# Kernel tuning notes

Measured on AMD Instinct MI355X. Metric: run time of the kernel, lower is better.

## Reference

```python
import jax, jax.numpy as jnp
import numpy as np

SLICES = (512, 32, 0, 8, 40, 72, 104, 136, 168, 200, 232, 264, 296)


def _build_params(slices):
    (d_in, w_pos, st_, sym1_, sym2_, pos1_, pos2_, pos3_,
     scr1_, scr2_, scr3_, scr4_, scr5_) = slices
    w_q = np.zeros((w_pos + 1, d_in), np.float32)
    b_q = -np.ones(w_pos + 1, np.float32)
    w_q[np.arange(w_pos), pos3_ + np.arange(w_pos)] = 2.0
    b_q[w_pos] = 1.0
    w_k = np.zeros((w_pos + 1, d_in), np.float32)
    b_k = -np.ones(w_pos + 1, np.float32)
    w_k[np.arange(w_pos), pos1_ + np.arange(w_pos)] = 2.0
    b_k[w_pos] = 0.0
    w_v = np.zeros((d_in, d_in), np.float32)
    b_v = np.zeros(d_in, np.float32)
    n = scr3_ - scr2_
    w_v[scr2_ + np.arange(n), sym1_ + np.arange(n)] = 1.0
    b_v[scr4_ + 1] = 1.0
    k_0 = np.zeros(w_pos + 1, np.float32)
    k_0[w_pos] = float(w_pos - 1)
    v_0 = np.zeros(d_in, np.float32)
    return {k: jnp.asarray(v) for k, v in dict(
        w_q=w_q, b_q=b_q, w_k=w_k, b_k=b_k, w_v=w_v, b_v=b_v,
        k_0=k_0, v_0=v_0).items()}


def setup_inputs() -> dict:
    key = jax.random.key(0)
    k1, k2 = jax.random.split(key)
    B, T, S, d_in = 8, 2048, 2048, SLICES[0]
    inp = {
        'tgt': jax.random.normal(k1, (B, T, d_in), dtype=jnp.float32),
        'memory': jax.random.normal(k2, (B, S, d_in), dtype=jnp.float32),
    }
    inp.update(_build_params(SLICES))
    return inp


def reference(tgt, memory, w_q, b_q, w_k, b_k, w_v, b_v, k_0, v_0):
    # Single-head cross-attention with an extra constant (k_0, v_0) token,
    # followed by a residual add (tgt += attn_out).
    B = tgt.shape[0]
    q = tgt @ w_q.T + b_q            # [B, T, h]   h = w_pos + 1
    k = memory @ w_k.T + b_k         # [B, S, h]
    v = memory @ w_v.T + b_v         # [B, S, d_in]
    # prepend the fixed default key/value token
    k0 = jnp.broadcast_to(k_0, (B, 1, k_0.shape[0]))
    v0 = jnp.broadcast_to(v_0, (B, 1, v_0.shape[0]))
    k = jnp.concatenate([k0, k], axis=1)   # [B, S+1, h]
    v = jnp.concatenate([v0, v], axis=1)   # [B, S+1, d_in]
    scores = jnp.einsum('bth,bsh->bts', q, k)      # [B, T, S+1]
    attn = jax.nn.softmax(scores, axis=-1)
    out = jnp.einsum('bts,bsd->btd', attn, v)       # [B, T, d_in]
    return tgt + out
```

## Files before the change

kernel.cpp:

```cpp
#include <hip/hip_runtime.h>
#include <hip/hip_bf16.h>

#define B_   8
#define T_   2048
#define S_   2048
#define DIN  512
#define QOFF 136
#define KOFF 72
#define VSRC 8

typedef __attribute__((ext_vector_type(8))) short    bf16x8;
typedef __attribute__((ext_vector_type(8))) _Float16 f16x8;
typedef __attribute__((ext_vector_type(4))) float    f32x4;

constexpr int KSEC = 0;
constexpr int VSEC = 524288;
constexpr int BATCH_U = 65536;

constexpr int BLK = 256;
constexpr int NGW = 16;

__device__ __forceinline__ ushort f2b(float x) {
  __hip_bfloat16 h = __float2bfloat16(x);
  return __builtin_bit_cast(ushort, h);
}
__device__ __forceinline__ ushort f2h(float x) {
  return __builtin_bit_cast(ushort, (_Float16)x);
}

__global__ __launch_bounds__(256)
void preproc(const float* __restrict__ mem, ushort* __restrict__ ws) {
  const int t    = threadIdx.x;
  const int b    = blockIdx.x >> 5;
  const int key0 = (blockIdx.x & 31) * 64;
  const float*  mbase = mem + (size_t)b * S_ * DIN;
  ushort* wk = ws + KSEC + (size_t)b * BATCH_U;
  ushort* wv = ws + VSEC + (size_t)b * BATCH_U;

  #pragma unroll
  for (int rep = 0; rep < 2; ++rep) {
    const int cid = t + 256 * rep;
    const int key = cid >> 3, c = cid & 7;
    const float4 k4 = *(const float4*)(mbase + (size_t)(key0 + key) * DIN + KOFF + 4 * c);
    const float kf[4] = {k4.x, k4.y, k4.z, k4.w};
    ushort kh[4];
    #pragma unroll
    for (int e = 0; e < 4; ++e) kh[e] = f2h(2.f * kf[e] - 1.f);
    const int gkey = key0 + key;
    const int pos  = (gkey >> 4) * 512 + ((gkey & 15) + 16 * (c >> 1)) * 8 + 4 * (c & 1);
    *(uint2*)(wk + pos) = *(const uint2*)kh;
  }

  const int ch = t & 31, h = t >> 5;
  float vv[8];
  #pragma unroll
  for (int r = 0; r < 8; ++r)
    vv[r] = mbase[(size_t)(key0 + 8 * h + r) * DIN + VSRC + ch];
  ushort vb[8];
  #pragma unroll
  for (int r = 0; r < 8; ++r) vb[r] = f2b(vv[r]);
  #pragma unroll
  for (int half = 0; half < 2; ++half) {
    const int key = key0 + 8 * h + 4 * half;
    const int pos = (key >> 5) * 1024 + (ch >> 4) * 512
                  + ((ch & 15) + 16 * ((key >> 2) & 3)) * 8 + ((key >> 4) & 1) * 4;
    *(uint2*)(wv + pos) = *(const uint2*)&vb[half * 4];
  }
}

__device__ __forceinline__ void mwrite(float* d, int lane, float m, float ls,
                                       const f32x4& o0, const f32x4& o1) {
  d[lane] = m;
  d[64 + lane] = ls;
  #pragma unroll
  for (int i = 0; i < 4; ++i) {
    d[128 + i * 64 + lane] = o0[i];
    d[384 + i * 64 + lane] = o1[i];
  }
}
__device__ __forceinline__ void mread(const float* s, int lane, float& m,
                                      float& ls, f32x4& o0, f32x4& o1) {
  const float m1 = s[lane], l1 = s[64 + lane];
  const float mn = fmaxf(m, m1);
  const float sa = __expf(m - mn), sb = __expf(m1 - mn);
  ls = ls * sa + l1 * sb;
  #pragma unroll
  for (int i = 0; i < 4; ++i) {
    o0[i] = o0[i] * sa + s[128 + i * 64 + lane] * sb;
    o1[i] = o1[i] * sa + s[384 + i * 64 + lane] * sb;
  }
  m = mn;
}

__global__ __launch_bounds__(BLK, 4)
void attn_main(const float* __restrict__ tgt, const ushort* __restrict__ ws,
               float* __restrict__ out) {
  __shared__ float msl[3 * 640 + 561];

  const int tid  = threadIdx.x;
  const int lane = tid & 63;
  const int wv   = tid >> 6;
  const int Q    = lane >> 4;
  const int r15  = lane & 15;

  const int o  = (blockIdx.x & 7) * 128 + (blockIdx.x >> 3);
  const int b  = o >> 7;
  const int t0 = (o & 127) * 16;

  const ushort* wsK = ws + KSEC + (size_t)b * BATCH_U;
  const ushort* wsV = ws + VSEC + (size_t)b * BATCH_U;
  const size_t  base = (size_t)(b * T_ + t0) * DIN;

  const float* tr = tgt + base + (size_t)r15 * DIN + QOFF + 8 * Q;
  const float4 qa = *(const float4*)tr;
  const float4 qb = *(const float4*)(tr + 4);
  f16x8 pf;
  {
    const float pv[8] = {qa.x, qa.y, qa.z, qa.w, qb.x, qb.y, qb.z, qb.w};
    #pragma unroll
    for (int e = 0; e < 8; ++e) pf[e] = (_Float16)(2.f * pv[e] - 1.f);
  }

  float m  = 31.f;
  float ls = (Q == 0 && wv == 0) ? 1.f : 0.f;
  f32x4 oc0 = {0.f, 0.f, 0.f, 0.f}, oc1 = {0.f, 0.f, 0.f, 0.f};

  bf16x8 stg[2][4];
  #define ISSUE(g, pb)                                                         \
    { const int ki = (wv * 32 + 2 * (g)) * 512 + lane * 8;                     \
      stg[pb][0] = *(const bf16x8*)(wsK + ki);                                 \
      stg[pb][1] = *(const bf16x8*)(wsK + ki + 512);                           \
      const int vi = (wv * NGW + (g)) * 1024 + lane * 8;                       \
      stg[pb][2] = *(const bf16x8*)(wsV + vi);                                 \
      stg[pb][3] = *(const bf16x8*)(wsV + vi + 512); }

  f32x4 cp[2];
  int cpr[2], cpc[2];
  #define CLOAD(c, pb)                                                         \
    { const int vid = (c) * BLK + tid;                                         \
      cpr[pb] = vid >> 7; cpc[pb] = vid & 127;                                 \
      cp[pb] = *(const f32x4*)(tgt + base + (size_t)cpr[pb] * DIN + cpc[pb] * 4); }
  #define CSTORE(pb)                                                           \
    { const int cc = cpc[pb];                                                  \
      if (!((cc >= 50 && cc < 58) || cc == 66))                                \
        *(f32x4*)(out + base + (size_t)cpr[pb] * DIN + cc * 4) = cp[pb]; }

  ISSUE(0, 0)
  ISSUE(1, 1)
  CLOAD(0, 0)

  #pragma unroll
  for (int g = 0; g < NGW; ++g) {
    const int pb = g & 1;
    if (g >= 1 && g <= 8) CSTORE((g - 1) & 1)
    if (g >= 1 && g < 8)  CLOAD(g, g & 1)

    const f16x8  k0 = __builtin_bit_cast(f16x8, stg[pb][0]);
    const f16x8  k1 = __builtin_bit_cast(f16x8, stg[pb][1]);
    const bf16x8 v0 = stg[pb][2];
    const bf16x8 v1 = stg[pb][3];

    f32x4 c0 = {0.f, 0.f, 0.f, 0.f}, c1 = {0.f, 0.f, 0.f, 0.f};
    c0 = __builtin_amdgcn_mfma_f32_16x16x32_f16(k0, pf, c0, 0, 0, 0);
    c1 = __builtin_amdgcn_mfma_f32_16x16x32_f16(k1, pf, c1, 0, 0, 0);

    if (g + 2 < NGW) ISSUE(g + 2, pb)

    float gm = fmaxf(fmaxf(fmaxf(c0[0], c0[1]), fmaxf(c0[2], c0[3])),
                     fmaxf(fmaxf(c1[0], c1[1]), fmaxf(c1[2], c1[3])));
    gm = fmaxf(gm, __shfl_xor(gm, 16));
    gm = fmaxf(gm, __shfl_xor(gm, 32));
    if (__any(gm > m + 8.f)) {
      const float mn  = gm;
      const float scl = __expf(m - fmaxf(m, mn));
      const float mx  = fmaxf(m, mn);
      m = mx;
      ls *= scl;
      #pragma unroll
      for (int i = 0; i < 4; ++i) { oc0[i] *= scl; oc1[i] *= scl; }
    }

    bf16x8 wf;
    float wsum = 0.f;
    #pragma unroll
    for (int j = 0; j < 8; ++j) {
      const float w = __expf(((j < 4) ? c0[j & 3] : c1[j & 3]) - m);
      wsum += w;
      wf[j] = (short)f2b(w);
    }
    ls += wsum;

    oc0 = __builtin_amdgcn_mfma_f32_16x16x32_bf16(v0, wf, oc0, 0, 0, 0);
    oc1 = __builtin_amdgcn_mfma_f32_16x16x32_bf16(v1, wf, oc1, 0, 0, 0);
  }
  #undef ISSUE
  #undef CLOAD
  #undef CSTORE

  if (wv >= 2) mwrite(msl + (wv - 2) * 640, lane, m, ls, oc0, oc1);
  __syncthreads();
  if (wv < 2) mread(msl + wv * 640, lane, m, ls, oc0, oc1);
  __syncthreads();
  if (wv == 1) mwrite(msl, lane, m, ls, oc0, oc1);
  __syncthreads();
  float* olds = msl + 1920;
  if (wv == 0) {
    mread(msl, lane, m, ls, oc0, oc1);
    float t2 = ls + __shfl_xor(ls, 16);
    const float lt  = t2 + __shfl_xor(t2, 32);
    const float inv = 1.f / lt;
    #pragma unroll
    for (int i = 0; i < 4; ++i) {
      olds[(4 * Q + i) * 17 + r15]      = oc0[i] * inv;
      olds[(16 + 4 * Q + i) * 17 + r15] = oc1[i] * inv;
    }
    if (Q == 0) olds[32 * 17 + r15] = 1.f - __expf(31.f - m) * inv;
  }
  __syncthreads();

  if (tid < 144) {
    const int row = tid / 9, j = tid - row * 9;
    const int c4i = (j < 8) ? (50 + j) : 66;
    const size_t off = base + (size_t)row * DIN + c4i * 4;
    float4 ov = *(const float4*)(tgt + off);
    if (j < 8) {
      ov.x += olds[(4 * j + 0) * 17 + row];
      ov.y += olds[(4 * j + 1) * 17 + row];
      ov.z += olds[(4 * j + 2) * 17 + row];
      ov.w += olds[(4 * j + 3) * 17 + row];
    } else {
      ov.y += olds[32 * 17 + row];
    }
    *(float4*)(out + off) = ov;
  }
}

extern "C" void kernel_launch(void* const* d_in, const int* in_sizes, int n_in,
                              void* d_out, int out_size, void* d_ws, size_t ws_size,
                              hipStream_t stream) {
  const float* tgt = (const float*)d_in[0];
  const float* mem = (const float*)d_in[1];
  ushort* ws = (ushort*)d_ws;
  float* out = (float*)d_out;
  preproc<<<dim3(256), dim3(256), 0, stream>>>(mem, ws);
  attn_main<<<dim3(B_ * (T_ / 16)), dim3(BLK), 0, stream>>>(tgt, ws, out);
}
```

Baseline: 29.31 us.

## Process two 16-row query tiles per block to reuse K/V loads

Each block now handles 32 query rows as two 16-row tiles that share every K and V fragment loaded from the workspace. Per-tile online-softmax state (max, sum, accumulators) is duplicated, and the shared-memory merge and epilogue are extended to cover both tiles. The grid is halved and the copy-through of tgt to out is spread over all 16 iterations. This halves K/V global traffic per query row, at the cost of more registers, more LDS, and fewer blocks in flight.

```diff
diff --git a/kernel.cpp b/kernel.cpp
--- a/kernel.cpp
+++ b/kernel.cpp
@@ -68,34 +68,43 @@
   }
 }
 
-__device__ __forceinline__ void mwrite(float* d, int lane, float m, float ls,
-                                       const f32x4& o0, const f32x4& o1) {
-  d[lane] = m;
-  d[64 + lane] = ls;
-  #pragma unroll
-  for (int i = 0; i < 4; ++i) {
-    d[128 + i * 64 + lane] = o0[i];
-    d[384 + i * 64 + lane] = o1[i];
-  }
-}
-__device__ __forceinline__ void mread(const float* s, int lane, float& m,
-                                      float& ls, f32x4& o0, f32x4& o1) {
-  const float m1 = s[lane], l1 = s[64 + lane];
-  const float mn = fmaxf(m, m1);
-  const float sa = __expf(m - mn), sb = __expf(m1 - mn);
-  ls = ls * sa + l1 * sb;
-  #pragma unroll
-  for (int i = 0; i < 4; ++i) {
-    o0[i] = o0[i] * sa + s[128 + i * 64 + lane] * sb;
-    o1[i] = o1[i] * sa + s[384 + i * 64 + lane] * sb;
-  }
-  m = mn;
+__device__ __forceinline__ void mwrite(float* d, int lane, const float* m,
+                                       const float* ls, const f32x4 o0[2],
+                                       const f32x4 o1[2]) {
+  #pragma unroll
+  for (int rt = 0; rt < 2; ++rt) {
+    float* dr = d + rt * 640;
+    dr[lane] = m[rt];
+    dr[64 + lane] = ls[rt];
+    #pragma unroll
+    for (int i = 0; i < 4; ++i) {
+      dr[128 + i * 64 + lane] = o0[rt][i];
+      dr[384 + i * 64 + lane] = o1[rt][i];
+    }
+  }
+}
+__device__ __forceinline__ void mread(const float* s, int lane, float* m,
+                                      float* ls, f32x4 o0[2], f32x4 o1[2]) {
+  #pragma unroll
+  for (int rt = 0; rt < 2; ++rt) {
+    const float* sr = s + rt * 640;
+    const float m1 = sr[lane], l1 = sr[64 + lane];
+    const float mn = fmaxf(m[rt], m1);
+    const float sa = __expf(m[rt] - mn), sb = __expf(m1 - mn);
+    ls[rt] = ls[rt] * sa + l1 * sb;
+    #pragma unroll
+    for (int i = 0; i < 4; ++i) {
+      o0[rt][i] = o0[rt][i] * sa + sr[128 + i * 64 + lane] * sb;
+      o1[rt][i] = o1[rt][i] * sa + sr[384 + i * 64 + lane] * sb;
+    }
+    m[rt] = mn;
+  }
 }
 
 __global__ __launch_bounds__(BLK, 4)
 void attn_main(const float* __restrict__ tgt, const ushort* __restrict__ ws,
                float* __restrict__ out) {
-  __shared__ float msl[3 * 640 + 561];
+  __shared__ float msl[3 * 1280 + 2 * 561];
 
   const int tid  = threadIdx.x;
   const int lane = tid & 63;
@@ -103,27 +112,30 @@
   const int Q    = lane >> 4;
   const int r15  = lane & 15;
 
-  const int o  = (blockIdx.x & 7) * 128 + (blockIdx.x >> 3);
-  const int b  = o >> 7;
-  const int t0 = (o & 127) * 16;
+  const int o  = (blockIdx.x & 7) * 64 + (blockIdx.x >> 3);
+  const int b  = o >> 6;
+  const int t0 = (o & 63) * 32;
 
   const ushort* wsK = ws + KSEC + (size_t)b * BATCH_U;
   const ushort* wsV = ws + VSEC + (size_t)b * BATCH_U;
   const size_t  base = (size_t)(b * T_ + t0) * DIN;
 
-  const float* tr = tgt + base + (size_t)r15 * DIN + QOFF + 8 * Q;
-  const float4 qa = *(const float4*)tr;
-  const float4 qb = *(const float4*)(tr + 4);
-  f16x8 pf;
-  {
+  f16x8 pf[2];
+  #pragma unroll
+  for (int rt = 0; rt < 2; ++rt) {
+    const float* tr = tgt + base + (size_t)(rt * 16 + r15) * DIN + QOFF + 8 * Q;
+    const float4 qa = *(const float4*)tr;
+    const float4 qb = *(const float4*)(tr + 4);
     const float pv[8] = {qa.x, qa.y, qa.z, qa.w, qb.x, qb.y, qb.z, qb.w};
     #pragma unroll
-    for (int e = 0; e < 8; ++e) pf[e] = (_Float16)(2.f * pv[e] - 1.f);
-  }
-
-  float m  = 31.f;
-  float ls = (Q == 0 && wv == 0) ? 1.f : 0.f;
-  f32x4 oc0 = {0.f, 0.f, 0.f, 0.f}, oc1 = {0.f, 0.f, 0.f, 0.f};
+    for (int e = 0; e < 8; ++e) pf[rt][e] = (_Float16)(2.f * pv[e] - 1.f);
+  }
+
+  float m[2]  = {31.f, 31.f};
+  float ls[2];
+  ls[0] = ls[1] = (Q == 0 && wv == 0) ? 1.f : 0.f;
+  f32x4 oc0[2] = {{0.f, 0.f, 0.f, 0.f}, {0.f, 0.f, 0.f, 0.f}};
+  f32x4 oc1[2] = {{0.f, 0.f, 0.f, 0.f}, {0.f, 0.f, 0.f, 0.f}};
 
   bf16x8 stg[2][4];
   #define ISSUE(g, pb)                                                         \
@@ -152,86 +164,98 @@
   #pragma unroll
   for (int g = 0; g < NGW; ++g) {
     const int pb = g & 1;
-    if (g >= 1 && g <= 8) CSTORE((g - 1) & 1)
-    if (g >= 1 && g < 8)  CLOAD(g, g & 1)
+    if (g >= 1)           CSTORE((g - 1) & 1)
+    if (g >= 1 && g < 16) CLOAD(g, g & 1)
 
     const f16x8  k0 = __builtin_bit_cast(f16x8, stg[pb][0]);
     const f16x8  k1 = __builtin_bit_cast(f16x8, stg[pb][1]);
     const bf16x8 v0 = stg[pb][2];
     const bf16x8 v1 = stg[pb][3];
 
-    f32x4 c0 = {0.f, 0.f, 0.f, 0.f}, c1 = {0.f, 0.f, 0.f, 0.f};
-    c0 = __builtin_amdgcn_mfma_f32_16x16x32_f16(k0, pf, c0, 0, 0, 0);
-    c1 = __builtin_amdgcn_mfma_f32_16x16x32_f16(k1, pf, c1, 0, 0, 0);
-
     if (g + 2 < NGW) ISSUE(g + 2, pb)
 
-    float gm = fmaxf(fmaxf(fmaxf(c0[0], c0[1]), fmaxf(c0[2], c0[3])),
-                     fmaxf(fmaxf(c1[0], c1[1]), fmaxf(c1[2], c1[3])));
-    gm = fmaxf(gm, __shfl_xor(gm, 16));
-    gm = fmaxf(gm, __shfl_xor(gm, 32));
-    if (__any(gm > m + 8.f)) {
-      const float mn  = gm;
-      const float scl = __expf(m - fmaxf(m, mn));
-      const float mx  = fmaxf(m, mn);
-      m = mx;
-      ls *= scl;
+    #pragma unroll
+    for (int rt = 0; rt < 2; ++rt) {
+      f32x4 c0 = {0.f, 0.f, 0.f, 0.f}, c1 = {0.f, 0.f, 0.f, 0.f};
+      c0 = __builtin_amdgcn_mfma_f32_16x16x32_f16(k0, pf[rt], c0, 0, 0, 0);
+      c1 = __builtin_amdgcn_mfma_f32_16x16x32_f16(k1, pf[rt], c1, 0, 0, 0);
+
+      float gm = fmaxf(fmaxf(fmaxf(c0[0], c0[1]), fmaxf(c0[2], c0[3])),
+                       fmaxf(fmaxf(c1[0], c1[1]), fmaxf(c1[2], c1[3])));
+      gm = fmaxf(gm, __shfl_xor(gm, 16));
+      gm = fmaxf(gm, __shfl_xor(gm, 32));
+      if (__any(gm > m[rt] + 8.f)) {
+        const float mn  = gm;
+        const float scl = __expf(m[rt] - fmaxf(m[rt], mn));
+        const float mx  = fmaxf(m[rt], mn);
+        m[rt] = mx;
+        ls[rt] *= scl;
+        #pragma unroll
+        for (int i = 0; i < 4; ++i) { oc0[rt][i] *= scl; oc1[rt][i] *= scl; }
+      }
+
+      bf16x8 wf;
+      float wsum = 0.f;
       #pragma unroll
-      for (int i = 0; i < 4; ++i) { oc0[i] *= scl; oc1[i] *= scl; }
-    }
-
-    bf16x8 wf;
-    float wsum = 0.f;
-    #pragma unroll
-    for (int j = 0; j < 8; ++j) {
-      const float w = __expf(((j < 4) ? c0[j & 3] : c1[j & 3]) - m);
-      wsum += w;
-      wf[j] = (short)f2b(w);
-    }
-    ls += wsum;
-
-    oc0 = __builtin_amdgcn_mfma_f32_16x16x32_bf16(v0, wf, oc0, 0, 0, 0);
-    oc1 = __builtin_amdgcn_mfma_f32_16x16x32_bf16(v1, wf, oc1, 0, 0, 0);
-  }
+      for (int j = 0; j < 8; ++j) {
+        const float w = __expf(((j < 4) ? c0[j & 3] : c1[j & 3]) - m[rt]);
+        wsum += w;
+        wf[j] = (short)f2b(w);
+      }
+      ls[rt] += wsum;
+
+      oc0[rt] = __builtin_amdgcn_mfma_f32_16x16x32_bf16(v0, wf, oc0[rt], 0, 0, 0);
+      oc1[rt] = __builtin_amdgcn_mfma_f32_16x16x32_bf16(v1, wf, oc1[rt], 0, 0, 0);
+    }
+  }
+  CSTORE(15 & 1)
   #undef ISSUE
   #undef CLOAD
   #undef CSTORE
 
-  if (wv >= 2) mwrite(msl + (wv - 2) * 640, lane, m, ls, oc0, oc1);
-  __syncthreads();
-  if (wv < 2) mread(msl + wv * 640, lane, m, ls, oc0, oc1);
+  if (wv >= 2) mwrite(msl + (wv - 2) * 1280, lane, m, ls, oc0, oc1);
+  __syncthreads();
+  if (wv < 2) mread(msl + wv * 1280, lane, m, ls, oc0, oc1);
   __syncthreads();
   if (wv == 1) mwrite(msl, lane, m, ls, oc0, oc1);
   __syncthreads();
-  float* olds = msl + 1920;
+  float* olds = msl + 3 * 1280;
   if (wv == 0) {
     mread(msl, lane, m, ls, oc0, oc1);
-    float t2 = ls + __shfl_xor(ls, 16);
-    const float lt  = t2 + __shfl_xor(t2, 32);
-    const float inv = 1.f / lt;
-    #pragma unroll
-    for (int i = 0; i < 4; ++i) {
-      olds[(4 * Q + i) * 17 + r15]      = oc0[i] * inv;
-      olds[(16 + 4 * Q + i) * 17 + r15] = oc1[i] * inv;
-    }
-    if (Q == 0) olds[32 * 17 + r15] = 1.f - __expf(31.f - m) * inv;
-  }
-  __syncthreads();
-
-  if (tid < 144) {
-    const int row = tid / 9, j = tid - row * 9;
-    const int c4i = (j < 8) ? (50 + j) : 66;
-    const size_t off = base + (size_t)row * DIN + c4i * 4;
-    float4 ov = *(const float4*)(tgt + off);
-    if (j < 8) {
-      ov.x += olds[(4 * j + 0) * 17 + row];
-      ov.y += olds[(4 * j + 1) * 17 + row];
-      ov.z += olds[(4 * j + 2) * 17 + row];
-      ov.w += olds[(4 * j + 3) * 17 + row];
-    } else {
-      ov.y += olds[32 * 17 + row];
-    }
-    *(float4*)(out + off) = ov;
+    #pragma unroll
+    for (int rt = 0; rt < 2; ++rt) {
+      float t2 = ls[rt] + __shfl_xor(ls[rt], 16);
+      const float lt  = t2 + __shfl_xor(t2, 32);
+      const float inv = 1.f / lt;
+      #pragma unroll
+      for (int i = 0; i < 4; ++i) {
+        olds[rt * 561 + (4 * Q + i) * 17 + r15]      = oc0[rt][i] * inv;
+        olds[rt * 561 + (16 + 4 * Q + i) * 17 + r15] = oc1[rt][i] * inv;
+      }
+      if (Q == 0) olds[rt * 561 + 32 * 17 + r15] = 1.f - __expf(31.f - m[rt]) * inv;
+    }
+  }
+  __syncthreads();
+
+  #pragma unroll
+  for (int k = 0; k < 2; ++k) {
+    const int idx = tid + k * BLK;
+    if (idx < 288) {
+      const int row = idx / 9, j = idx - row * 9;
+      const int rt = row >> 4, rr = row & 15;
+      const int c4i = (j < 8) ? (50 + j) : 66;
+      const size_t off = base + (size_t)row * DIN + c4i * 4;
+      float4 ov = *(const float4*)(tgt + off);
+      if (j < 8) {
+        ov.x += olds[rt * 561 + (4 * j + 0) * 17 + rr];
+        ov.y += olds[rt * 561 + (4 * j + 1) * 17 + rr];
+        ov.z += olds[rt * 561 + (4 * j + 2) * 17 + rr];
+        ov.w += olds[rt * 561 + (4 * j + 3) * 17 + rr];
+      } else {
+        ov.y += olds[rt * 561 + 32 * 17 + rr];
+      }
+      *(float4*)(out + off) = ov;
+    }
   }
 }
 
@@ -243,5 +267,5 @@
   ushort* ws = (ushort*)d_ws;
   float* out = (float*)d_out;
   preproc<<<dim3(256), dim3(256), 0, stream>>>(mem, ws);
-  attn_main<<<dim3(B_ * (T_ / 16)), dim3(BLK), 0, stream>>>(tgt, ws, out);
-}
+  attn_main<<<dim3(B_ * (T_ / 32)), dim3(BLK), 0, stream>>>(tgt, ws, out);
+}
```

After: 27.53 us, median of 2. 6.1% less time.
